# Kernel tuning notes

Hardware: AMD Instinct MI355X
Metric: run time of the kernel (lower is better)

Reference implementation:

```python
import jax, jax.numpy as jnp
import numpy as np

EPSILON = 1e-10
T, N, IN_DIM = 50, 2048, 16   # seq_len, num_stocks, lstm input dims
R, K, H = 8, 32, 128          # relations, max neighbors, lstm hidden dims


def setup_inputs() -> dict:
    key = jax.random.key(0)
    ks = jax.random.split(key, 10)
    s = 1.0 / np.sqrt(H)
    stock_hist = jax.random.normal(ks[0], (T, N, IN_DIM), dtype=jnp.float32)
    neighbors = jax.random.randint(ks[1], (R, N, K), 0, N + 1, dtype=jnp.int32)
    # rel_num: count of real (nonzero) neighbors per relation per stock
    rel_num = jnp.sum(neighbors != 0, axis=-1).astype(jnp.float32)  # [R, N]
    return {
        "stock_hist": stock_hist,
        "neighbors": neighbors,
        "rel_num": rel_num,
        # LSTM params (torch gate order i,f,g,o)
        "W_ih": jax.random.normal(ks[2], (4 * H, IN_DIM), dtype=jnp.float32) * s,
        "W_hh": jax.random.normal(ks[3], (4 * H, H), dtype=jnp.float32) * s,
        "b_ih": jnp.zeros((4 * H,), dtype=jnp.float32),
        "b_hh": jnp.zeros((4 * H,), dtype=jnp.float32),
        # fc_att: Linear(2H + R -> 1)
        "w_att": jax.random.normal(ks[4], (2 * H + R,), dtype=jnp.float32) * s,
        "b_att": jnp.zeros((), dtype=jnp.float32),
        # fc_rel_att: Linear(H + R -> 1)
        "w_rel": jax.random.normal(ks[5], (H + R,), dtype=jnp.float32) * s,
        "b_rel": jnp.zeros((), dtype=jnp.float32),
        "w_fc1": jax.random.normal(ks[6], (H, 1), dtype=jnp.float32) * s,
        "b_fc1": jnp.zeros((1,), dtype=jnp.float32),
    }


def _lstm_final_h(x, W_ih, W_hh, b_ih, b_hh):
    # x: [T, N, In] -> final hidden state h_T: [N, H]
    n = x.shape[1]
    h0 = jnp.zeros((n, H), x.dtype)
    c0 = jnp.zeros((n, H), x.dtype)

    def step(carry, x_t):
        h, c = carry
        z = x_t @ W_ih.T + h @ W_hh.T + (b_ih + b_hh)
        i, f, g, o = jnp.split(z, 4, axis=-1)
        c = jax.nn.sigmoid(f) * c + jax.nn.sigmoid(i) * jnp.tanh(g)
        h = jax.nn.sigmoid(o) * jnp.tanh(c)
        return (h, c), None

    (h, _), _ = jax.lax.scan(step, (h0, c0), x)
    return h


def reference(stock_hist, neighbors, rel_num, W_ih, W_hh, b_ih, b_hh,
              w_att, b_att, w_rel, b_rel, w_fc1, b_fc1):
    se = _lstm_final_h(stock_hist, W_ih, W_hh, b_ih, b_hh)        # [N, H]
    se_pad = jnp.concatenate([jnp.zeros((1, H), se.dtype), se], 0)  # row 0 = padding

    # --- graph attention layer ---
    nb_emb = se_pad[neighbors]                                    # [R, N, K, H] gather
    # fc_att over concat(nb_emb, self_emb, one_hot(R)) == split-weight matvecs
    w_nb, w_self, w_oh = w_att[:H], w_att[H:2 * H], w_att[2 * H:]
    score = (nb_emb @ w_nb                                        # [R, N, K]
             + (se @ w_self)[None, :, None]                       # self emb broadcast
             + w_oh[:, None, None]                                # one-hot relation emb
             + b_att)
    att_w = jax.nn.softmax(score, axis=2)                         # softmax over neighbors
    rel_rep = jnp.einsum('rnk,rnkh->rnh', att_w, nb_emb) / (rel_num + EPSILON)[..., None]

    # fc_rel_att over concat(rel_rep, one_hot(R))
    wr_h, wr_oh = w_rel[:H], w_rel[H:]
    rscore = rel_rep @ wr_h + wr_oh[:, None] + b_rel              # [R, N]
    rel_w = jax.nn.softmax(rscore, axis=0)                        # softmax over relations
    updated = jnp.mean(rel_w[..., None] * rel_rep, axis=0)        # [N, H]

    final = updated + se                                          # residual (state_embedding[1:])
    preds = final @ w_fc1 + b_fc1
    return preds
```

## Files before the change

### kernel.cpp

```cpp
#include <hip/hip_runtime.h>
#include <math.h>

#define T_STEPS 50
#define NS      2048
#define IND     16
#define HID     128
#define GATES   512
#define RR      8
#define KN      32
#define EPSV    1e-10f

#define LROWS   8
#define APAD    168
#define LTH     512

typedef _Float16 f16x8 __attribute__((ext_vector_type(8)));
typedef _Float16 f16x4 __attribute__((ext_vector_type(4)));
typedef float    f32x4 __attribute__((ext_vector_type(4)));

__device__ __forceinline__ float rcp_(float x)  { return __builtin_amdgcn_rcpf(x); }
__device__ __forceinline__ float sigm(float x)  { return rcp_(1.0f + __expf(-x)); }
__device__ __forceinline__ float tanhf_(float x){ return 1.0f - 2.0f * rcp_(1.0f + __expf(2.0f * x)); }

__device__ __forceinline__ f16x8 zero8() {
    f16x8 z;
#pragma unroll
    for (int j = 0; j < 8; ++j) z[j] = (_Float16)0.0f;
    return z;
}

__global__ __launch_bounds__(LTH, 2) void lstm_mfma_kernel(
    const float* __restrict__ x,
    const float* __restrict__ W_ih,
    const float* __restrict__ W_hh,
    const float* __restrict__ b_ih,
    const float* __restrict__ b_hh,
    float* __restrict__ se,
    _Float16* __restrict__ se16)
{
    __shared__ __align__(16) _Float16 sA[2][LROWS][APAD];
    __shared__ __align__(16) _Float16 sX[T_STEPS][LROWS * IND];

    const int tid    = threadIdx.x;
    const int w      = tid >> 6;
    const int l      = tid & 63;
    const int lane16 = l & 15;
    const int lgrp   = l >> 4;
    const int n0     = blockIdx.x * LROWS;

    f16x8 B[4][5];
    float bias[4];
#pragma unroll
    for (int gg = 0; gg < 4; ++gg) {
        const int gi = 128 * gg + 16 * w + lane16;
        bias[gg] = b_ih[gi] + b_hh[gi];
#pragma unroll
        for (int kf = 0; kf < 5; ++kf) {
            const int k0 = kf * 32 + lgrp * 8;
            f16x8 v;
            if (k0 < 16) {
                const float* p = W_ih + gi * IND + k0;
#pragma unroll
                for (int j = 0; j < 8; ++j) v[j] = (_Float16)p[j];
            } else if (k0 >= 144) {
                v = zero8();
            } else {
                const float* p = W_hh + gi * HID + (k0 - 16);
#pragma unroll
                for (int j = 0; j < 8; ++j) v[j] = (_Float16)p[j];
            }
            B[gg][kf] = v;
        }
    }
#pragma unroll
    for (int gg = 0; gg < 4; ++gg)
#pragma unroll
        for (int kf = 0; kf < 5; ++kf)
            asm volatile("" : "+v"(B[gg][kf]));

    for (int i = tid; i < 2 * LROWS * APAD; i += LTH)
        (&sA[0][0][0])[i] = (_Float16)0.0f;

    for (int i = tid; i < T_STEPS * LROWS * IND; i += LTH) {
        const int t = i >> 7, e = i & 127;
        sX[t][e] = (_Float16)x[((size_t)t * NS + n0) * IND + e];
    }
    __syncthreads();
    if (tid < LROWS * IND) sA[0][tid >> 4][tid & 15] = sX[0][tid];
    __syncthreads();

    const bool evenrow = (lane16 & 1) == 0;
    const int  arow    = lane16 >> 1;
    float c0 = 0.f, c1 = 0.f, h0 = 0.f, h1 = 0.f;

    for (int step = 0; step < T_STEPS; ++step) {
        const int cur = step & 1, nxt = cur ^ 1;

        f16x8 A[5];
#pragma unroll
        for (int kf = 0; kf < 5; ++kf) {
            f16x8 v = zero8();
            if (evenrow)
                v = *(const f16x8*)&sA[cur][arow][kf * 32 + lgrp * 8];
            A[kf] = v;
        }

        _Float16 xv = (_Float16)0.0f;
        if (step + 1 < T_STEPS && tid < LROWS * IND) xv = sX[step + 1][tid];

        f32x4 zi = {bias[0], bias[0], bias[0], bias[0]};
        f32x4 zf = {bias[1], bias[1], bias[1], bias[1]};
        f32x4 zg = {bias[2], bias[2], bias[2], bias[2]};
        f32x4 zo = {bias[3], bias[3], bias[3], bias[3]};
#pragma unroll
        for (int kf = 0; kf < 5; ++kf) {
            zi = __builtin_amdgcn_mfma_f32_16x16x32_f16(A[kf], B[0][kf], zi, 0, 0, 0);
            zf = __builtin_amdgcn_mfma_f32_16x16x32_f16(A[kf], B[1][kf], zf, 0, 0, 0);
            zg = __builtin_amdgcn_mfma_f32_16x16x32_f16(A[kf], B[2][kf], zg, 0, 0, 0);
            zo = __builtin_amdgcn_mfma_f32_16x16x32_f16(A[kf], B[3][kf], zo, 0, 0, 0);
        }

        c0 = sigm(zf[0]) * c0 + sigm(zi[0]) * tanhf_(zg[0]);
        h0 = sigm(zo[0]) * tanhf_(c0);
        c1 = sigm(zf[2]) * c1 + sigm(zi[2]) * tanhf_(zg[2]);
        h1 = sigm(zo[2]) * tanhf_(c1);

        if (step + 1 < T_STEPS) {
            if (tid < LROWS * IND) sA[nxt][tid >> 4][tid & 15] = xv;
            sA[nxt][2 * lgrp][16 + 16 * w + lane16]     = (_Float16)h0;
            sA[nxt][2 * lgrp + 1][16 + 16 * w + lane16] = (_Float16)h1;
        }
        __syncthreads();
    }

    se[(n0 + 2 * lgrp) * HID + 16 * w + lane16]     = h0;
    se[(n0 + 2 * lgrp + 1) * HID + 16 * w + lane16] = h1;
    se16[(n0 + 2 * lgrp) * HID + 16 * w + lane16]     = (_Float16)h0;
    se16[(n0 + 2 * lgrp + 1) * HID + 16 * w + lane16] = (_Float16)h1;
}

__global__ __launch_bounds__(256) void precompute_kernel(
    const float* __restrict__ se,
    const float* __restrict__ w_att,
    float* __restrict__ sw,
    float* __restrict__ p2n)
{
    const int wid  = threadIdx.x >> 6;
    const int lane = threadIdx.x & 63;
    const int n    = blockIdx.x * 4 + wid;

    const float a = se[n * HID + lane];
    const float b = se[n * HID + 64 + lane];
    float d1 = a * w_att[lane]       + b * w_att[64 + lane];
    float d2 = a * w_att[HID + lane] + b * w_att[HID + 64 + lane];
#pragma unroll
    for (int d = 32; d > 0; d >>= 1) {
        d1 += __shfl_xor(d1, d);
        d2 += __shfl_xor(d2, d);
    }
    if (lane == 0) { sw[n] = d1; p2n[n] = d2; }
}

__global__ __launch_bounds__(512) void attn_fused_kernel(
    const _Float16* __restrict__ se16,
    const float* __restrict__ se,
    const int*   __restrict__ neighbors,
    const float* __restrict__ rel_num,
    const float* __restrict__ sw,
    const float* __restrict__ p2n,
    const float* __restrict__ w_att,
    const float* __restrict__ b_att,
    const float* __restrict__ w_rel,
    const float* __restrict__ b_rel,
    const float* __restrict__ w_fc1,
    const float* __restrict__ b_fc1,
    float* __restrict__ out)
{
    __shared__ float srel[RR][HID];
    __shared__ float srsc[RR];

    const int r    = threadIdx.x >> 6;
    const int lane = threadIdx.x & 63;
    const int n    = blockIdx.x;
    const size_t pair = (size_t)r * NS + n;
    const f16x4* se16_4 = (const f16x4*)se16;

    int myidx = 0;
    if (lane < KN) myidx = neighbors[pair * KN + lane];

    float s = 0.f;
    if (lane < KN) {
        float swv = (myidx != 0) ? sw[myidx - 1] : 0.f;
        s = swv + p2n[n] + w_att[2 * HID + r] + b_att[0];
    }
    float mx = s;
#pragma unroll
    for (int d = 16; d > 0; d >>= 1) mx = fmaxf(mx, __shfl_xor(mx, d, 32));
    float e  = __expf(s - mx);
    float sm = e;
#pragma unroll
    for (int d = 16; d > 0; d >>= 1) sm += __shfl_xor(sm, d, 32);
    float att = e * rcp_(sm);

    const int k2 = lane >> 5;
    const int c4 = lane & 31;
    float ax = 0.f, ay = 0.f, az = 0.f, aw = 0.f;
#pragma unroll
    for (int kk = 0; kk < KN / 2; ++kk) {
        const int   kq = kk * 2 + k2;
        const float av = __shfl(att, kq);
        const int  idq = __shfl(myidx, kq);
        if (idq != 0) {
            f16x4 v = se16_4[(size_t)(idq - 1) * (HID / 4) + c4];
            ax += av * (float)v[0]; ay += av * (float)v[1];
            az += av * (float)v[2]; aw += av * (float)v[3];
        }
    }
    ax += __shfl_xor(ax, 32); ay += __shfl_xor(ay, 32);
    az += __shfl_xor(az, 32); aw += __shfl_xor(aw, 32);

    const float inv = rcp_(rel_num[pair] + EPSV);
    float pr = 0.f;
    if (k2 == 0) {
        ax *= inv; ay *= inv; az *= inv; aw *= inv;
        *(float4*)&srel[r][c4 * 4] = make_float4(ax, ay, az, aw);
        pr = ax * w_rel[c4 * 4] + ay * w_rel[c4 * 4 + 1]
           + az * w_rel[c4 * 4 + 2] + aw * w_rel[c4 * 4 + 3];
    }
#pragma unroll
    for (int d = 16; d > 0; d >>= 1) pr += __shfl_xor(pr, d, 32);
    if (lane == 0) srsc[r] = pr + w_rel[HID + r] + b_rel[0];

    __syncthreads();

    if (r == 0) {
        float rs[RR];
        float rmx = -1e30f;
#pragma unroll
        for (int q = 0; q < RR; ++q) {
            rs[q] = srsc[q];
            rmx = fmaxf(rmx, rs[q]);
        }
        float rsm = 0.f;
#pragma unroll
        for (int q = 0; q < RR; ++q) {
            rs[q] = __expf(rs[q] - rmx);
            rsm += rs[q];
        }
        const float invs = rcp_(rsm * (float)RR);

        float u0 = 0.f, u1 = 0.f;
#pragma unroll
        for (int q = 0; q < RR; ++q) {
            u0 += rs[q] * srel[q][lane];
            u1 += rs[q] * srel[q][64 + lane];
        }
        u0 = u0 * invs + se[n * HID + lane];
        u1 = u1 * invs + se[n * HID + 64 + lane];

        float p = u0 * w_fc1[lane] + u1 * w_fc1[64 + lane];
#pragma unroll
        for (int d = 32; d > 0; d >>= 1) p += __shfl_xor(p, d);
        if (lane == 0) out[n] = p + b_fc1[0];
    }
}

extern "C" void kernel_launch(void* const* d_in, const int* in_sizes, int n_in,
                              void* d_out, int out_size, void* d_ws, size_t ws_size,
                              hipStream_t stream) {
    const float* x      = (const float*)d_in[0];
    const int*   nbrs   = (const int*)  d_in[1];
    const float* relnum = (const float*)d_in[2];
    const float* W_ih   = (const float*)d_in[3];
    const float* W_hh   = (const float*)d_in[4];
    const float* b_ih   = (const float*)d_in[5];
    const float* b_hh   = (const float*)d_in[6];
    const float* w_att  = (const float*)d_in[7];
    const float* b_att  = (const float*)d_in[8];
    const float* w_rel  = (const float*)d_in[9];
    const float* b_rel  = (const float*)d_in[10];
    const float* w_fc1  = (const float*)d_in[11];
    const float* b_fc1  = (const float*)d_in[12];
    float* out = (float*)d_out;

    float*    se   = (float*)d_ws;
    _Float16* se16 = (_Float16*)(se + (size_t)NS * HID);
    float*    sw   = (float*)(se16 + (size_t)NS * HID);
    float*    p2n  = sw + NS;

    hipLaunchKernelGGL(lstm_mfma_kernel, dim3(NS / LROWS), dim3(LTH), 0, stream,
                       x, W_ih, W_hh, b_ih, b_hh, se, se16);
    hipLaunchKernelGGL(precompute_kernel, dim3(NS / 4), dim3(256), 0, stream,
                       se, w_att, sw, p2n);
    hipLaunchKernelGGL(attn_fused_kernel, dim3(NS), dim3(512), 0, stream,
                       se16, se, nbrs, relnum, sw, p2n, w_att, b_att,
                       w_rel, b_rel, w_fc1, b_fc1, out);
}
```

Measured before the change: 70.98 us.

## Halve LSTM rows per block to double block count and parallelism

Each LSTM block now handles 4 stocks instead of 8, so twice as many blocks run the serial 50-step recurrence. A-matrix rows are spaced every 4th row of a 16-row zero-padded tile, and each lane computes one cell instead of two. This spreads the latency-bound recurrence over more CUs, at the cost of loading the W fragments into registers in twice as many blocks and leaving more of each MFMA tile as zero padding. The launch grid must also scale with the new LROWS.

```diff
diff --git a/kernel.cpp b/kernel.cpp
--- a/kernel.cpp
+++ b/kernel.cpp
@@ -10,7 +10,7 @@
 #define KN      32
 #define EPSV    1e-10f
 
-#define LROWS   8
+#define LROWS   4
 #define APAD    168
 #define LTH     512
 
@@ -38,7 +38,7 @@
     float* __restrict__ se,
     _Float16* __restrict__ se16)
 {
-    __shared__ __align__(16) _Float16 sA[2][LROWS][APAD];
+    __shared__ __align__(16) _Float16 sA[2][16][APAD];
     __shared__ __align__(16) _Float16 sX[T_STEPS][LROWS * IND];
 
     const int tid    = threadIdx.x;
@@ -78,32 +78,26 @@
         for (int kf = 0; kf < 5; ++kf)
             asm volatile("" : "+v"(B[gg][kf]));
 
-    for (int i = tid; i < 2 * LROWS * APAD; i += LTH)
+    for (int i = tid; i < 2 * 16 * APAD; i += LTH)
         (&sA[0][0][0])[i] = (_Float16)0.0f;
 
     for (int i = tid; i < T_STEPS * LROWS * IND; i += LTH) {
-        const int t = i >> 7, e = i & 127;
+        const int t = i >> 6, e = i & 63;
         sX[t][e] = (_Float16)x[((size_t)t * NS + n0) * IND + e];
     }
     __syncthreads();
-    if (tid < LROWS * IND) sA[0][tid >> 4][tid & 15] = sX[0][tid];
+    if (tid < LROWS * IND) sA[0][4 * (tid >> 4)][tid & 15] = sX[0][tid];
     __syncthreads();
 
-    const bool evenrow = (lane16 & 1) == 0;
-    const int  arow    = lane16 >> 1;
-    float c0 = 0.f, c1 = 0.f, h0 = 0.f, h1 = 0.f;
+    float c = 0.f, h = 0.f;
 
     for (int step = 0; step < T_STEPS; ++step) {
         const int cur = step & 1, nxt = cur ^ 1;
 
         f16x8 A[5];
 #pragma unroll
-        for (int kf = 0; kf < 5; ++kf) {
-            f16x8 v = zero8();
-            if (evenrow)
-                v = *(const f16x8*)&sA[cur][arow][kf * 32 + lgrp * 8];
-            A[kf] = v;
-        }
+        for (int kf = 0; kf < 5; ++kf)
+            A[kf] = *(const f16x8*)&sA[cur][lane16][kf * 32 + lgrp * 8];
 
         _Float16 xv = (_Float16)0.0f;
         if (step + 1 < T_STEPS && tid < LROWS * IND) xv = sX[step + 1][tid];
@@ -120,23 +114,18 @@
             zo = __builtin_amdgcn_mfma_f32_16x16x32_f16(A[kf], B[3][kf], zo, 0, 0, 0);
         }
 
-        c0 = sigm(zf[0]) * c0 + sigm(zi[0]) * tanhf_(zg[0]);
-        h0 = sigm(zo[0]) * tanhf_(c0);
-        c1 = sigm(zf[2]) * c1 + sigm(zi[2]) * tanhf_(zg[2]);
-        h1 = sigm(zo[2]) * tanhf_(c1);
+        c = sigm(zf[0]) * c + sigm(zi[0]) * tanhf_(zg[0]);
+        h = sigm(zo[0]) * tanhf_(c);
 
         if (step + 1 < T_STEPS) {
-            if (tid < LROWS * IND) sA[nxt][tid >> 4][tid & 15] = xv;
-            sA[nxt][2 * lgrp][16 + 16 * w + lane16]     = (_Float16)h0;
-            sA[nxt][2 * lgrp + 1][16 + 16 * w + lane16] = (_Float16)h1;
+            if (tid < LROWS * IND) sA[nxt][4 * (tid >> 4)][tid & 15] = xv;
+            sA[nxt][4 * lgrp][16 + 16 * w + lane16] = (_Float16)h;
         }
         __syncthreads();
     }
 
-    se[(n0 + 2 * lgrp) * HID + 16 * w + lane16]     = h0;
-    se[(n0 + 2 * lgrp + 1) * HID + 16 * w + lane16] = h1;
-    se16[(n0 + 2 * lgrp) * HID + 16 * w + lane16]     = (_Float16)h0;
-    se16[(n0 + 2 * lgrp + 1) * HID + 16 * w + lane16] = (_Float16)h1;
+    se[(n0 + lgrp) * HID + 16 * w + lane16]   = h;
+    se16[(n0 + lgrp) * HID + 16 * w + lane16] = (_Float16)h;
 }
 
 __global__ __launch_bounds__(256) void precompute_kernel(
```

Result: slower. 93.91 us (+32.3%).
